# Performance work log

Hardware: AMD Instinct MI355X
Metric: run time of the kernel (lower is better)

Reference implementation:

```python
import jax, jax.numpy as jnp
import numpy as np

N = 1_000_000      # neurons
E = 16_000_000     # connections (edges)
NIN = 1024         # input vector length
NOUT = 8192        # output neurons gathered
REFRACTORY = 0.33  # config['refractory_factor']
CLIP = 1.0         # config['relu_clip_at']
NUM_ACTS = 8       # identity, relu, leaky_relu, clipped_relu, tanh, sigmoid, softplus, abs


def setup_inputs() -> dict:
    key = jax.random.key(0)
    ks = jax.random.split(key, 10)
    state = jax.random.normal(ks[0], (N,), dtype=jnp.float32)
    weights = jax.random.normal(ks[1], (E,), dtype=jnp.float32) * 0.1
    biases = jax.random.normal(ks[2], (N,), dtype=jnp.float32) * 0.1
    inp = jax.random.normal(ks[3], (NIN,), dtype=jnp.float32)
    src = jax.random.randint(ks[4], (E,), 0, N, dtype=jnp.int32)
    dst = jax.random.randint(ks[5], (E,), 0, N, dtype=jnp.int32)
    rec_mask = jax.random.randint(ks[6], (E,), 0, 2, dtype=jnp.int32).astype(bool)
    input_idx = jax.random.randint(ks[7], (E,), 0, NIN, dtype=jnp.int32)
    act_id = jax.random.randint(ks[8], (N,), 0, NUM_ACTS, dtype=jnp.int32)
    out_ids = jax.random.randint(ks[9], (NOUT,), 0, N, dtype=jnp.int32)
    return {"state": state, "weights": weights, "biases": biases, "inp": inp,
            "src": src, "dst": dst, "rec_mask": rec_mask,
            "input_idx": input_idx, "act_id": act_id, "out_ids": out_ids}


def _apply_activations(x, act_id):
    # Per-neuron activation select; ids follow ActivationFunctions order.
    acts = jnp.stack([
        x,                                   # identity
        jax.nn.relu(x),                      # relu
        jax.nn.leaky_relu(x),                # leaky_relu (default slope 0.01)
        jnp.clip(x, 0.0, CLIP),              # clipped_relu
        jnp.tanh(x),                         # tanh
        jax.nn.sigmoid(x),                   # sigmoid
        jax.nn.softplus(x),                  # softplus
        jnp.abs(x),                          # abs
    ])  # [8, N]
    return acts[act_id, jnp.arange(x.shape[0])]


def reference(state, weights, biases, inp, src, dst, rec_mask, input_idx, act_id, out_ids):
    # Shallow dict copy + in-place *= in torch scales the accumulation base too.
    prev = REFRACTORY * state                                    # [N]
    # Per-edge source value: recurrent edges read prev state, others read input.
    from_state = jnp.where(rec_mask, prev[src], inp[input_idx])  # [E]
    msg = weights * from_state                                   # [E]
    acc = prev + jax.ops.segment_sum(msg, dst, num_segments=N) + biases  # [N]
    new_state = _apply_activations(acc, act_id)                  # [N]
    return new_state[out_ids]                                    # [NOUT]
```

## Files before the change

### kernel.cpp

```cpp
#include <hip/hip_runtime.h>
#include <math.h>

#define REFRACTORY 0.33f
#define FILT_WORDS 32768
#define QWCAP 128
#define NWAVES 16
#define DRAIN_THRESH 16

#define WS_ACC_OFF 256

__global__ void setup(const unsigned int* __restrict__ rm, int nwords,
                      int* __restrict__ flag,
                      const int* __restrict__ out_ids,
                      const float* __restrict__ state,
                      const float* __restrict__ biases,
                      float* __restrict__ acc, int nout) {
    if (blockIdx.x == 0) {
        __shared__ int s;
        if (threadIdx.x == 0) s = 0;
        __syncthreads();
        int found = 0;
        for (int i = threadIdx.x; i < nwords; i += blockDim.x)
            if (rm[i] > 1u) found = 1;
        if (found) atomicOr(&s, 1);
        __syncthreads();
        if (threadIdx.x == 0) *flag = s;
    } else {
        int i = (blockIdx.x - 1) * blockDim.x + threadIdx.x;
        if (i < nout) {
            int n = out_ids[i];
            acc[n] = REFRACTORY * state[n] + biases[n];
        }
    }
}

__device__ __forceinline__ void process_edge(
    int d, int e,
    const float* __restrict__ w, const int* __restrict__ src,
    const unsigned char* __restrict__ rmb, const int* __restrict__ input_idx,
    const float* __restrict__ state, const float* __restrict__ inp,
    float* __restrict__ acc, int bytemode) {
    int m = bytemode ? (int)rmb[e] : ((const int*)rmb)[e];
    float v = m ? REFRACTORY * state[src[e]] : inp[input_idx[e]];
    unsafeAtomicAdd(&acc[d], w[e] * v);
}

__global__ void __launch_bounds__(1024, 1)
edge_fused(const int* __restrict__ dst,
           const int* __restrict__ out_ids, int nout,
           int E, int shift,
           const float* __restrict__ w, const int* __restrict__ src,
           const unsigned char* __restrict__ rmb,
           const int* __restrict__ input_idx,
           const float* __restrict__ state, const float* __restrict__ inp,
           float* __restrict__ acc,
           const int* __restrict__ flag) {
    __shared__ unsigned int filt[FILT_WORDS];
    __shared__ int2 lq[NWAVES * QWCAP];
    __shared__ int wcnt[NWAVES];

    {
        uint4* f4 = (uint4*)filt;
        uint4 z = make_uint4(0, 0, 0, 0);
        for (int i = threadIdx.x; i < FILT_WORDS / 4; i += blockDim.x)
            f4[i] = z;
    }
    if ((threadIdx.x & 63) == 0) wcnt[threadIdx.x >> 6] = 0;
    __syncthreads();
    for (int i = threadIdx.x; i < nout; i += blockDim.x) {
        unsigned g = ((unsigned)out_ids[i]) >> shift;
        atomicOr(&filt[g >> 5], 1u << (g & 31));
    }
    __syncthreads();

    const int bytemode = *flag;
    const int lane = threadIdx.x & 63;
    const int wv = threadIdx.x >> 6;
    int2* wq = &lq[wv * QWCAP];
    int* mycnt = &wcnt[wv];

    int gtid = blockIdx.x * blockDim.x + threadIdx.x;
    int gstride = gridDim.x * blockDim.x;
    int nq = E >> 2;
    const int4* d4p = (const int4*)dst;

#define PROBE(dv, hv, k)                                                       \
    { unsigned dd = (unsigned)(dv) >> shift;                                   \
      hv |= ((filt[dd >> 5] >> (dd & 31)) & 1u) << (k); }

#define ENQ(ev, dv)                                                            \
    { int off = atomicAdd(mycnt, 1);                                           \
      if (off < QWCAP) wq[off] = make_int2((ev), (int)(dv));                   \
      else process_edge((int)(dv), (ev), w, src, rmb, input_idx,               \
                        state, inp, acc, bytemode); }

    for (int t = gtid; t < nq; t += 2 * gstride) {
        int tB = t + gstride;
        bool vB = tB < nq;
        int4 A = d4p[t];
        int4 B = vB ? d4p[tB] : make_int4(0, 0, 0, 0);

        unsigned mA = 0, mB = 0;
        PROBE(A.x, mA, 0) PROBE(A.y, mA, 1) PROBE(A.z, mA, 2) PROBE(A.w, mA, 3)
        PROBE(B.x, mB, 0) PROBE(B.y, mB, 1) PROBE(B.z, mB, 2) PROBE(B.w, mB, 3)
        if (!vB) mB = 0;

        if (mA | mB) {
            int ea = t << 2, eb = tB << 2;
            if (mA & 1) ENQ(ea + 0, A.x)
            if (mA & 2) ENQ(ea + 1, A.y)
            if (mA & 4) ENQ(ea + 2, A.z)
            if (mA & 8) ENQ(ea + 3, A.w)
            if (mB & 1) ENQ(eb + 0, B.x)
            if (mB & 2) ENQ(eb + 1, B.y)
            if (mB & 4) ENQ(eb + 2, B.z)
            if (mB & 8) ENQ(eb + 3, B.w)
        }

        int have = *mycnt;
        if (have >= DRAIN_THRESH) {
            int nn = have < QWCAP ? have : QWCAP;
            for (int i = lane; i < nn; i += 64) {
                int2 c = wq[i];
                process_edge(c.y, c.x, w, src, rmb, input_idx,
                             state, inp, acc, bytemode);
            }
            if (lane == 0) *mycnt = 0;
        }
    }
#undef PROBE
#undef ENQ

    int rem = E - nq * 4;
    if (gtid < rem) {
        int e = nq * 4 + gtid;
        int d = dst[e];
        process_edge(d, e, w, src, rmb, input_idx, state, inp, acc, bytemode);
    }

    {
        int have = *mycnt;
        int nn = have < QWCAP ? have : QWCAP;
        for (int i = lane; i < nn; i += 64) {
            int2 c = wq[i];
            process_edge(c.y, c.x, w, src, rmb, input_idx,
                         state, inp, acc, bytemode);
        }
    }
}

__global__ void gather_out(const float* __restrict__ acc,
                           const int* __restrict__ act_id,
                           const int* __restrict__ out_ids,
                           float* __restrict__ out, int nout) {
    int i = blockIdx.x * blockDim.x + threadIdx.x;
    if (i >= nout) return;
    int n = out_ids[i];
    float x = acc[n];
    float y;
    switch (act_id[n]) {
        case 0: y = x; break;
        case 1: y = fmaxf(x, 0.0f); break;
        case 2: y = x > 0.0f ? x : 0.01f * x; break;
        case 3: y = fminf(fmaxf(x, 0.0f), 1.0f); break;
        case 4: y = tanhf(x); break;
        case 5: y = 1.0f / (1.0f + expf(-x)); break;
        case 6: y = fmaxf(x, 0.0f) + log1pf(expf(-fabsf(x))); break;
        default: y = fabsf(x); break;
    }
    out[i] = y;
}

extern "C" void kernel_launch(void* const* d_in, const int* in_sizes, int n_in,
                              void* d_out, int out_size, void* d_ws, size_t ws_size,
                              hipStream_t stream) {
    const float* state     = (const float*)d_in[0];
    const float* weights   = (const float*)d_in[1];
    const float* biases    = (const float*)d_in[2];
    const float* inp       = (const float*)d_in[3];
    const int*   src       = (const int*)d_in[4];
    const int*   dst       = (const int*)d_in[5];
    const void*  rec_mask  = d_in[6];
    const int*   input_idx = (const int*)d_in[7];
    const int*   act_id    = (const int*)d_in[8];
    const int*   out_ids   = (const int*)d_in[9];
    float*       out       = (float*)d_out;

    const int N = in_sizes[0];
    const int E = in_sizes[1];
    const int NOUT = out_size;

    int*   flag = (int*)d_ws;
    float* acc  = (float*)((char*)d_ws + WS_ACC_OFF);

    int shift = 0;
    while ((((long long)N + ((1LL << shift) - 1)) >> shift) > (long long)FILT_WORDS * 32)
        shift++;

    int nwords = E / 4;
    if (nwords > 2048) nwords = 2048;
    if (nwords < 1) nwords = 1;
    int setupBlocks = 1 + (NOUT + 255) / 256;
    setup<<<setupBlocks, 256, 0, stream>>>((const unsigned int*)rec_mask, nwords,
                                           flag, out_ids, state, biases, acc, NOUT);

    edge_fused<<<256, 1024, 0, stream>>>(
        dst, out_ids, NOUT, E, shift,
        weights, src, (const unsigned char*)rec_mask, input_idx,
        state, inp, acc, flag);

    gather_out<<<(NOUT + 255) / 256, 256, 0, stream>>>(acc, act_id, out_ids, out, NOUT);
}
```

Measured before the change: 37.79 us.

## Split waves into filter producers and a dedicated consumer wave via shared queue

Replaces the per-wave local queues, which each wave drained itself, with a producer/consumer scheme. Fifteen waves scan dst, probe the shared-memory bitmap filter and push hits into one block-wide LDS queue. The sixteenth wave spins on that queue and performs the gather and atomic-add work. The aim is to overlap the long-latency gathers with the streaming scan. The costs are one-sixteenth less scan bandwidth, spin-waiting, and contention on a single atomic counter. Once the queue of 1024 entries fills, producers fall back to processing edges inline.

Result: slower. 44.14 us (+16.8%).

```diff
diff --git a/kernel.cpp b/kernel.cpp
--- a/kernel.cpp
+++ b/kernel.cpp
@@ -3,9 +3,8 @@
 
 #define REFRACTORY 0.33f
 #define FILT_WORDS 32768
-#define QWCAP 128
-#define NWAVES 16
-#define DRAIN_THRESH 16
+#define QCAP 1024
+#define NPROD 15
 
 #define WS_ACC_OFF 256
 
@@ -56,8 +55,9 @@
            float* __restrict__ acc,
            const int* __restrict__ flag) {
     __shared__ unsigned int filt[FILT_WORDS];
-    __shared__ int2 lq[NWAVES * QWCAP];
-    __shared__ int wcnt[NWAVES];
+    __shared__ int qd[QCAP];
+    __shared__ int qe[QCAP];
+    __shared__ int wr, rd, done;
 
     {
         uint4* f4 = (uint4*)filt;
@@ -65,7 +65,8 @@
         for (int i = threadIdx.x; i < FILT_WORDS / 4; i += blockDim.x)
             f4[i] = z;
     }
-    if ((threadIdx.x & 63) == 0) wcnt[threadIdx.x >> 6] = 0;
+    for (int i = threadIdx.x; i < QCAP; i += blockDim.x) qe[i] = 0;
+    if (threadIdx.x == 0) { wr = 0; rd = 0; done = 0; }
     __syncthreads();
     for (int i = threadIdx.x; i < nout; i += blockDim.x) {
         unsigned g = ((unsigned)out_ids[i]) >> shift;
@@ -76,74 +77,78 @@
     const int bytemode = *flag;
     const int lane = threadIdx.x & 63;
     const int wv = threadIdx.x >> 6;
-    int2* wq = &lq[wv * QWCAP];
-    int* mycnt = &wcnt[wv];
-
-    int gtid = blockIdx.x * blockDim.x + threadIdx.x;
-    int gstride = gridDim.x * blockDim.x;
-    int nq = E >> 2;
-    const int4* d4p = (const int4*)dst;
+
+    if (wv < NPROD) {
+        int pgid = blockIdx.x * (NPROD * 64) + wv * 64 + lane;
+        int pstride = gridDim.x * (NPROD * 64);
+        int nq = E >> 2;
+        const int4* d4p = (const int4*)dst;
 
 #define PROBE(dv, hv, k)                                                       \
     { unsigned dd = (unsigned)(dv) >> shift;                                   \
       hv |= ((filt[dd >> 5] >> (dd & 31)) & 1u) << (k); }
 
 #define ENQ(ev, dv)                                                            \
-    { int off = atomicAdd(mycnt, 1);                                           \
-      if (off < QWCAP) wq[off] = make_int2((ev), (int)(dv));                   \
-      else process_edge((int)(dv), (ev), w, src, rmb, input_idx,               \
-                        state, inp, acc, bytemode); }
-
-    for (int t = gtid; t < nq; t += 2 * gstride) {
-        int tB = t + gstride;
-        bool vB = tB < nq;
-        int4 A = d4p[t];
-        int4 B = vB ? d4p[tB] : make_int4(0, 0, 0, 0);
-
-        unsigned mA = 0, mB = 0;
-        PROBE(A.x, mA, 0) PROBE(A.y, mA, 1) PROBE(A.z, mA, 2) PROBE(A.w, mA, 3)
-        PROBE(B.x, mB, 0) PROBE(B.y, mB, 1) PROBE(B.z, mB, 2) PROBE(B.w, mB, 3)
-        if (!vB) mB = 0;
-
-        if (mA | mB) {
-            int ea = t << 2, eb = tB << 2;
-            if (mA & 1) ENQ(ea + 0, A.x)
-            if (mA & 2) ENQ(ea + 1, A.y)
-            if (mA & 4) ENQ(ea + 2, A.z)
-            if (mA & 8) ENQ(ea + 3, A.w)
-            if (mB & 1) ENQ(eb + 0, B.x)
-            if (mB & 2) ENQ(eb + 1, B.y)
-            if (mB & 4) ENQ(eb + 2, B.z)
-            if (mB & 8) ENQ(eb + 3, B.w)
-        }
-
-        int have = *mycnt;
-        if (have >= DRAIN_THRESH) {
-            int nn = have < QWCAP ? have : QWCAP;
-            for (int i = lane; i < nn; i += 64) {
-                int2 c = wq[i];
-                process_edge(c.y, c.x, w, src, rmb, input_idx,
-                             state, inp, acc, bytemode);
+    { int off = atomicAdd(&wr, 1);                                             \
+      if (off < QCAP) {                                                        \
+          qd[off] = (int)(dv);                                                 \
+          __threadfence_block();                                               \
+          qe[off] = (ev) + 1;                                                  \
+      } else process_edge((int)(dv), (ev), w, src, rmb, input_idx,             \
+                          state, inp, acc, bytemode); }
+
+        for (int t = pgid; t < nq; t += 2 * pstride) {
+            int tB = t + pstride;
+            bool vB = tB < nq;
+            int4 A = d4p[t];
+            int4 B = vB ? d4p[tB] : make_int4(0, 0, 0, 0);
+
+            unsigned mA = 0, mB = 0;
+            PROBE(A.x, mA, 0) PROBE(A.y, mA, 1) PROBE(A.z, mA, 2) PROBE(A.w, mA, 3)
+            PROBE(B.x, mB, 0) PROBE(B.y, mB, 1) PROBE(B.z, mB, 2) PROBE(B.w, mB, 3)
+            if (!vB) mB = 0;
+
+            if (mA | mB) {
+                int ea = t << 2, eb = tB << 2;
+                if (mA & 1) ENQ(ea + 0, A.x)
+                if (mA & 2) ENQ(ea + 1, A.y)
+                if (mA & 4) ENQ(ea + 2, A.z)
+                if (mA & 8) ENQ(ea + 3, A.w)
+                if (mB & 1) ENQ(eb + 0, B.x)
+                if (mB & 2) ENQ(eb + 1, B.y)
+                if (mB & 4) ENQ(eb + 2, B.z)
+                if (mB & 8) ENQ(eb + 3, B.w)
             }
-            if (lane == 0) *mycnt = 0;
-        }
-    }
+        }
 #undef PROBE
 #undef ENQ
 
-    int rem = E - nq * 4;
-    if (gtid < rem) {
-        int e = nq * 4 + gtid;
-        int d = dst[e];
-        process_edge(d, e, w, src, rmb, input_idx, state, inp, acc, bytemode);
-    }
-
-    {
-        int have = *mycnt;
-        int nn = have < QWCAP ? have : QWCAP;
-        for (int i = lane; i < nn; i += 64) {
-            int2 c = wq[i];
-            process_edge(c.y, c.x, w, src, rmb, input_idx,
+        int rem = E - nq * 4;
+        if (pgid < rem) {
+            int e = nq * 4 + pgid;
+            int d = dst[e];
+            process_edge(d, e, w, src, rmb, input_idx, state, inp, acc, bytemode);
+        }
+
+        __threadfence_block();
+        if (lane == 0) atomicAdd(&done, 1);
+    } else {
+        volatile int* vqe = (volatile int*)qe;
+        volatile int* vwr = (volatile int*)&wr;
+        volatile int* vdone = (volatile int*)&done;
+        while (true) {
+            int idx = atomicAdd(&rd, 1);
+            if (idx >= QCAP) break;
+            int ev;
+            bool live = true;
+            while ((ev = vqe[idx]) == 0) {
+                if (*vdone == NPROD && *vwr <= idx) { live = false; break; }
+                __builtin_amdgcn_s_sleep(2);
+            }
+            if (!live) break;
+            __threadfence_block();
+            int d = qd[idx];
+            process_edge(d, ev - 1, w, src, rmb, input_idx,
                          state, inp, acc, bytemode);
         }
     }
```
